# Kernel tuning notes

Measured on AMD Instinct MI355X. Metric: run time of the kernel, lower is better.

The kernel has to match this reference:

```python
import jax, jax.numpy as jnp
import numpy as np

B, T, HID = 2, 2048, 2048
NH, NKV, HD = 32, 8, 64
SCALE = HD ** -0.5
ROPE_THETA = 10000.0


def _rope_tables(key):
    # standard HF llama rope: cos/sin of shape [B, T, head_dim]
    inv_freq = 1.0 / (ROPE_THETA ** (jnp.arange(0, HD, 2, dtype=jnp.float32) / HD))
    pos = jnp.arange(T, dtype=jnp.float32)
    freqs = pos[:, None] * inv_freq[None, :]            # [T, HD/2]
    emb = jnp.concatenate([freqs, freqs], axis=-1)      # [T, HD]
    cos = jnp.broadcast_to(jnp.cos(emb)[None], (B, T, HD))
    sin = jnp.broadcast_to(jnp.sin(emb)[None], (B, T, HD))
    return cos, sin


def setup_inputs() -> dict:
    key = jax.random.key(0)
    ks = jax.random.split(key, 5)
    hidden_states = jax.random.normal(ks[0], (B, T, HID), dtype=jnp.float32)
    cos, sin = _rope_tables(key)
    s = 0.02
    wq = jax.random.normal(ks[1], (NH * HD, HID), dtype=jnp.float32) * s
    wk = jax.random.normal(ks[2], (NKV * HD, HID), dtype=jnp.float32) * s
    wv = jax.random.normal(ks[3], (NKV * HD, HID), dtype=jnp.float32) * s
    wo = jax.random.normal(ks[4], (HID, NH * HD), dtype=jnp.float32) * s
    return {"hidden_states": hidden_states, "cos": cos, "sin": sin,
            "wq": wq, "wk": wk, "wv": wv, "wo": wo}


def _rotate_half(x):
    x1, x2 = jnp.split(x, 2, axis=-1)
    return jnp.concatenate([-x2, x1], axis=-1)


def _apply_rope(q, k, cos, sin):
    # q: [B, NH, T, HD], k: [B, NKV, T, HD]; cos/sin: [B, T, HD] -> unsqueeze head dim
    c = cos[:, None, :, :]
    s = sin[:, None, :, :]
    q = q * c + _rotate_half(q) * s
    k = k * c + _rotate_half(k) * s
    return q, k


def reference(hidden_states, cos, sin, wq, wk, wv, wo):
    b, t, _ = hidden_states.shape
    # QKV projections (no bias, llama-style)
    q = (hidden_states @ wq.T).reshape(b, t, NH, HD).transpose(0, 2, 1, 3)    # [B,NH,T,HD]
    k = (hidden_states @ wk.T).reshape(b, t, NKV, HD).transpose(0, 2, 1, 3)   # [B,NKV,T,HD]
    v = (hidden_states @ wv.T).reshape(b, t, NKV, HD).transpose(0, 2, 1, 3)
    q, k = _apply_rope(q, k, cos, sin)
    # GQA: repeat kv heads
    rep = NH // NKV
    k = jnp.repeat(k, rep, axis=1)   # [B,NH,T,HD]
    v = jnp.repeat(v, rep, axis=1)
    # causal attention, scaling = head_dim**-0.5
    logits = jnp.einsum("bhqd,bhkd->bhqk", q, k) * SCALE
    causal = jnp.tril(jnp.ones((t, t), dtype=bool))
    logits = jnp.where(causal[None, None], logits, jnp.finfo(logits.dtype).min)
    probs = jax.nn.softmax(logits, axis=-1)
    attn = jnp.einsum("bhqk,bhkd->bhqd", probs, v)       # [B,NH,T,HD]
    attn = attn.transpose(0, 2, 1, 3).reshape(b, t, NH * HD)
    return attn @ wo.T
```

## Files before the change

### kernel.cpp

```cpp
#include <hip/hip_runtime.h>
#include <hip/hip_bf16.h>

#define T_SEQ 2048
#define HID_DIM 2048

typedef __attribute__((ext_vector_type(8))) short short8;
typedef __attribute__((ext_vector_type(4))) short short4v;
typedef __attribute__((ext_vector_type(4))) float f32x4;

#define MFMA16(a, b, c) __builtin_amdgcn_mfma_f32_16x16x32_bf16((a), (b), (c), 0, 0, 0)

static __device__ __forceinline__ ushort f2bf(float f) {
  union { __hip_bfloat16 h; ushort u; } un;
  un.h = __float2bfloat16(f);
  return un.u;
}
static __device__ __forceinline__ float bf2f(ushort u) {
  union { ushort u; __hip_bfloat16 h; } un;
  un.u = u;
  return __bfloat162float(un.h);
}

static __device__ __forceinline__ void gload_lds16(const void* g, void* l) {
  __builtin_amdgcn_global_load_lds(
      (const __attribute__((address_space(1))) void*)g,
      (__attribute__((address_space(3))) void*)l, 16, 0, 0);
}

__global__ __launch_bounds__(256) void cast_kernel(const float* __restrict__ in,
                                                   ushort* __restrict__ out, int n4) {
  int i = blockIdx.x * 256 + threadIdx.x;
  if (i >= n4) return;
  const float4 v = reinterpret_cast<const float4*>(in)[i];
  ushort4 o;
  o.x = f2bf(v.x); o.y = f2bf(v.y); o.z = f2bf(v.z); o.w = f2bf(v.w);
  reinterpret_cast<ushort4*>(out)[i] = o;
}

__device__ __forceinline__ void store_c(float* p, float v) { *p = v; }
__device__ __forceinline__ void store_c(ushort* p, float v) { *p = f2bf(v); }

template <int MODE, int BN, typename OutT>
__global__ __launch_bounds__(512) void gemm8p(const ushort* __restrict__ A,
                                              const ushort* __restrict__ W,
                                              OutT* __restrict__ C,
                                              ushort* __restrict__ vTout,
                                              int M, int N, int K) {
  constexpr int LA = 4;
  constexpr int LB = BN / 64;
  constexpr int NR = BN / 64;
  __shared__ __align__(16) ushort As[2][256 * 64];
  __shared__ __align__(16) ushort Bs[2][BN * 64];
  const int tid = threadIdx.x;
  const int lane = tid & 63, l15 = lane & 15, lhi = lane >> 4;
  const int wid = tid >> 6, wm = wid >> 2, wn = wid & 3;
  const int brow = blockIdx.y * 256, bcol = blockIdx.x * BN;
  const int nkt = K >> 6;

  const ushort* asrc[LA]; ushort* adst[LA];
#pragma unroll
  for (int j = 0; j < LA; ++j) {
    const int c = tid + 512 * j, row = c >> 3, k16 = c & 7;
    asrc[j] = A + (size_t)(brow + row) * K + ((k16 ^ (row & 7)) << 3);
    adst[j] = &As[0][0] + c * 8;
  }
  const ushort* bsrc[LB]; ushort* bdst[LB];
#pragma unroll
  for (int j = 0; j < LB; ++j) {
    const int c = tid + 512 * j, row = c >> 3, k16 = c & 7;
    bsrc[j] = W + (size_t)(bcol + row) * K + ((k16 ^ (row & 7)) << 3);
    bdst[j] = &Bs[0][0] + c * 8;
  }

#define STAGE8(kt_, bf_) do {                                              \
    _Pragma("unroll")                                                      \
    for (int j = 0; j < LA; ++j)                                           \
      gload_lds16(asrc[j] + (kt_) * 64, adst[j] + (bf_) * (256 * 64));     \
    _Pragma("unroll")                                                      \
    for (int j = 0; j < LB; ++j)                                           \
      gload_lds16(bsrc[j] + (kt_) * 64, bdst[j] + (bf_) * (BN * 64));      \
  } while (0)

  f32x4 acc[8][NR] = {};

  STAGE8(0, 0);
  for (int kt = 0; kt < nkt; ++kt) {
    const int bf = kt & 1;
    if (kt + 1 < nkt) {
      STAGE8(kt + 1, bf ^ 1);
      if constexpr (LA + LB == 8) asm volatile("s_waitcnt vmcnt(8)" ::: "memory");
      else                        asm volatile("s_waitcnt vmcnt(6)" ::: "memory");
    } else {
      asm volatile("s_waitcnt vmcnt(0)" ::: "memory");
    }
    __builtin_amdgcn_s_barrier();
    const char* abuf = (const char*)&As[bf][0];
    const char* bbuf = (const char*)&Bs[bf][0];
#pragma unroll
    for (int mh = 0; mh < 2; ++mh) {
      short8 af[4][2];
#pragma unroll
      for (int mi = 0; mi < 4; ++mi) {
        const int row = wm * 128 + (mh * 4 + mi) * 16 + l15;
        const int sw = (row & 7) << 4;
#pragma unroll
        for (int ks = 0; ks < 2; ++ks)
          af[mi][ks] = *(const short8*)(abuf + row * 128 + ((ks * 64 + lhi * 16) ^ sw));
      }
#pragma unroll
      for (int nh = 0; nh < NR / 2; ++nh) {
        short8 bfrag[2][2];
#pragma unroll
        for (int ni = 0; ni < 2; ++ni) {
          const int rowb = wn * (BN / 4) + (nh * 2 + ni) * 16 + l15;
          const int sw = (rowb & 7) << 4;
#pragma unroll
          for (int ks = 0; ks < 2; ++ks)
            bfrag[ni][ks] = *(const short8*)(bbuf + rowb * 128 + ((ks * 64 + lhi * 16) ^ sw));
        }
        __builtin_amdgcn_s_setprio(1);
#pragma unroll
        for (int ks = 0; ks < 2; ++ks)
#pragma unroll
          for (int mi = 0; mi < 4; ++mi)
#pragma unroll
            for (int ni = 0; ni < 2; ++ni)
              acc[mh * 4 + mi][nh * 2 + ni] =
                  MFMA16(af[mi][ks], bfrag[ni][ks], acc[mh * 4 + mi][nh * 2 + ni]);
        __builtin_amdgcn_s_setprio(0);
      }
    }
    __builtin_amdgcn_s_barrier();
  }
#undef STAGE8

  if (MODE == 2 && bcol >= 2560) {
#pragma unroll
    for (int mi8 = 0; mi8 < 8; ++mi8) {
      const int row = brow + wm * 128 + mi8 * 16 + lhi * 4;
      const int bb = row >> 11, t = row & 2047;
#pragma unroll
      for (int ni = 0; ni < NR; ++ni) {
        const int cv = bcol + wn * (BN / 4) + ni * 16 + l15 - 2560;
        const int hk = cv >> 6, dd = cv & 63;
        ushort4 o;
        o.x = f2bf(acc[mi8][ni][0]); o.y = f2bf(acc[mi8][ni][1]);
        o.z = f2bf(acc[mi8][ni][2]); o.w = f2bf(acc[mi8][ni][3]);
        *(ushort4*)&vTout[(size_t)((bb * 8 + hk) * 64 + dd) * 2048 + t] = o;
      }
    }
  } else {
    const int cstride = (MODE == 2) ? 2560 : N;
#pragma unroll
    for (int mi8 = 0; mi8 < 8; ++mi8) {
      const int row = brow + wm * 128 + mi8 * 16 + lhi * 4;
#pragma unroll
      for (int ni = 0; ni < NR; ++ni) {
        const int col = bcol + wn * (BN / 4) + ni * 16 + l15;
#pragma unroll
        for (int r = 0; r < 4; ++r)
          store_c(&C[(size_t)(row + r) * cstride + col], acc[mi8][ni][r]);
      }
    }
  }
}

__global__ __launch_bounds__(256) void rope_kernel(ushort* __restrict__ qkv,
                                                   const float* __restrict__ ct,
                                                   const float* __restrict__ st) {
  const int bt = blockIdx.x;
  ushort* row = qkv + (size_t)bt * 2560;
  const float* c = ct + (size_t)bt * 64;
  const float* s = st + (size_t)bt * 64;
  const int tid = threadIdx.x;
#pragma unroll
  for (int it = 0; it < 5; ++it) {
    const int idx = it * 256 + tid;
    const bool isQ = idx < 1024;
    const int sub = isQ ? idx : idx - 1024;
    const int hh = sub >> 5;
    const int p = sub & 31;
    const int col = (isQ ? 0 : 2048) + hh * 64 + p;
    const float x1 = bf2f(row[col]);
    const float x2 = bf2f(row[col + 32]);
    const float cc = c[p], ss = s[p];
    float y1 = x1 * cc - x2 * ss;
    float y2 = x2 * cc + x1 * ss;
    if (isQ) { y1 *= 0.125f; y2 *= 0.125f; }
    row[col] = f2bf(y1);
    row[col + 32] = f2bf(y2);
  }
}

#define PROCESS(SUF, diag_) do {                                              \
    f32x4 s_[4] = {};                                                         \
    __builtin_amdgcn_s_setprio(1);                                            \
    _Pragma("unroll")                                                         \
    for (int n = 0; n < 4; ++n) {                                             \
      const short8 k0_ = *(const short8*)(KtB + n * 2048 + base0);            \
      const short8 k1_ = *(const short8*)(KtB + n * 2048 + base1);            \
      s_[n] = MFMA16(k0_, q##SUF##0, s_[n]);                                  \
      s_[n] = MFMA16(k1_, q##SUF##1, s_[n]);                                  \
    }                                                                         \
    __builtin_amdgcn_s_setprio(0);                                            \
    if (diag_) {                                                              \
      _Pragma("unroll")                                                       \
      for (int n = 0; n < 4; ++n) {                                           \
        const int kb_ = 16 * n + 4 * lhi;                                     \
        _Pragma("unroll")                                                     \
        for (int r = 0; r < 4; ++r)                                           \
          if (kb_ + r > qloc) s_[n][r] = -1e30f;                              \
      }                                                                       \
    }                                                                         \
    float mx_;                                                                \
    {                                                                         \
      const float m0_ = fmaxf(fmaxf(s_[0][0], s_[0][1]), fmaxf(s_[0][2], s_[0][3])); \
      const float m1_ = fmaxf(fmaxf(s_[1][0], s_[1][1]), fmaxf(s_[1][2], s_[1][3])); \
      const float m2_ = fmaxf(fmaxf(s_[2][0], s_[2][1]), fmaxf(s_[2][2], s_[2][3])); \
      const float m3_ = fmaxf(fmaxf(s_[3][0], s_[3][1]), fmaxf(s_[3][2], s_[3][3])); \
      mx_ = fmaxf(fmaxf(m0_, m1_), fmaxf(m2_, m3_));                          \
    }                                                                         \
    mx_ = fmaxf(mx_, __shfl_xor(mx_, 16));                                    \
    mx_ = fmaxf(mx_, __shfl_xor(mx_, 32));                                    \
    const float mn_ = fmaxf(mS##SUF, mx_);                                    \
    const float al_ = __expf(mS##SUF - mn_);                                  \
    _Pragma("unroll")                                                         \
    for (int n = 0; n < 4; ++n) {                                             \
      s_[n][0] = __expf(s_[n][0] - mn_);                                      \
      s_[n][1] = __expf(s_[n][1] - mn_);                                      \
      s_[n][2] = __expf(s_[n][2] - mn_);                                      \
      s_[n][3] = __expf(s_[n][3] - mn_);                                      \
    }                                                                         \
    float rs_;                                                                \
    {                                                                         \
      const float t0_ = (s_[0][0] + s_[0][1]) + (s_[0][2] + s_[0][3]);        \
      const float t1_ = (s_[1][0] + s_[1][1]) + (s_[1][2] + s_[1][3]);        \
      const float t2_ = (s_[2][0] + s_[2][1]) + (s_[2][2] + s_[2][3]);        \
      const float t3_ = (s_[3][0] + s_[3][1]) + (s_[3][2] + s_[3][3]);        \
      rs_ = (t0_ + t1_) + (t2_ + t3_);                                        \
    }                                                                         \
    rs_ += __shfl_xor(rs_, 16);                                               \
    rs_ += __shfl_xor(rs_, 32);                                               \
    lS##SUF = lS##SUF * al_ + rs_;                                            \
    mS##SUF = mn_;                                                            \
    _Pragma("unroll")                                                         \
    for (int n = 0; n < 4; ++n) {                                             \
      short4v pk_;                                                            \
      pk_[0] = (short)f2bf(s_[n][0]);                                         \
      pk_[1] = (short)f2bf(s_[n][1]);                                         \
      pk_[2] = (short)f2bf(s_[n][2]);                                         \
      pk_[3] = (short)f2bf(s_[n][3]);                                         \
      *(short4v*)(PtB + prow + 32 * n + 8 * lhi) = pk_;                       \
    }                                                                         \
    const float al0_ = __shfl(al_, 4 * lhi + 0);                              \
    const float al1_ = __shfl(al_, 4 * lhi + 1);                              \
    const float al2_ = __shfl(al_, 4 * lhi + 2);                              \
    const float al3_ = __shfl(al_, 4 * lhi + 3);                              \
    _Pragma("unroll")                                                         \
    for (int n = 0; n < 4; ++n) {                                             \
      o##SUF[n][0] *= al0_;                                                   \
      o##SUF[n][1] *= al1_;                                                   \
      o##SUF[n][2] *= al2_;                                                   \
      o##SUF[n][3] *= al3_;                                                   \
    }                                                                         \
    {                                                                         \
      const short8 p0_ = *(const short8*)(PtB + prow + 16 * lhi);             \
      const short8 p1_ = *(const short8*)(PtB + prow + 64 + 16 * lhi);        \
      __builtin_amdgcn_s_setprio(1);                                          \
      _Pragma("unroll")                                                       \
      for (int n = 0; n < 4; ++n) {                                           \
        const short8 v0_ = *(const short8*)(VtB + n * 2048 + base0);          \
        const short8 v1_ = *(const short8*)(VtB + n * 2048 + base1);          \
        o##SUF[n] = MFMA16(p0_, v0_, o##SUF[n]);                              \
        o##SUF[n] = MFMA16(p1_, v1_, o##SUF[n]);                              \
      }                                                                       \
      __builtin_amdgcn_s_setprio(0);                                          \
    }                                                                         \
  } while (0)

__global__ __launch_bounds__(256) void attn_kernel(const ushort* __restrict__ qkv,
                                                   const ushort* __restrict__ vT,
                                                   ushort* __restrict__ out) {
  __shared__ __align__(16) ushort Kt[4096];
  __shared__ __align__(16) ushort Vt[4096];
  __shared__ __align__(16) ushort Pt[64 * 72];
  const int bid = blockIdx.x;
  const int j = bid >> 3;
  const int bh = (bid & 7) * 8 + (j & 7);
  const int bx = j >> 3;
  const int b = bh >> 5, h = bh & 31, hkv = h >> 2;
  const int tid = threadIdx.x;
  const int wid = tid >> 6, lane = tid & 63, l15 = lane & 15, lhi = lane >> 4;
  const int qA = bx, qB = 31 - bx;
  const int qloc = wid * 16 + l15;

  short8 qA0, qA1, qB0, qB1;
  {
    const size_t offA = (size_t)(b * T_SEQ + qA * 64 + qloc) * 2560 + h * 64;
    qA0 = *(const short8*)(qkv + offA + lhi * 8);
    qA1 = *(const short8*)(qkv + offA + 32 + lhi * 8);
    const size_t offB = (size_t)(b * T_SEQ + qB * 64 + qloc) * 2560 + h * 64;
    qB0 = *(const short8*)(qkv + offB + lhi * 8);
    qB1 = *(const short8*)(qkv + offB + 32 + lhi * 8);
  }

  f32x4 oA[4] = {}, oB[4] = {};
  float mSA = -1e30f, lSA = 0.f, mSB = -1e30f, lSB = 0.f;

  const int swb = (l15 & 7) << 4;
  const int base0 = l15 * 128 + ((lhi * 16) ^ swb);
  const int base1 = l15 * 128 + ((64 + lhi * 16) ^ swb);
  const char* KtB = (const char*)Kt;
  const char* VtB = (const char*)Vt;
  char* PtB = (char*)Pt;
  const int prow = qloc * 144;

  const int srow = tid >> 3, sgrp = tid & 7;
  const int d0s = ((sgrp ^ (srow & 7)) * 8);
  const ushort* kb_g = qkv + (size_t)b * T_SEQ * 2560 + 2048 + hkv * 64;
  const ushort* vb_g = vT + (size_t)(b * 8 + hkv) * 64 * 2048;
  ushort* ldsK = Kt + tid * 8;
  ushort* ldsV = Vt + tid * 8;

  for (int kt = 0; kt <= qB; ++kt) {
    const int ktb = kt * 64;
    gload_lds16(kb_g + (size_t)(ktb + srow) * 2560 + d0s, ldsK);
    gload_lds16(kb_g + (size_t)(ktb + 32 + srow) * 2560 + d0s, ldsK + 2048);
    gload_lds16(vb_g + (size_t)srow * 2048 + ktb + d0s, ldsV);
    gload_lds16(vb_g + (size_t)(32 + srow) * 2048 + ktb + d0s, ldsV + 2048);
    __syncthreads();
    PROCESS(B, kt == qB);
    if (kt <= qA) PROCESS(A, kt == qA);
    __syncthreads();
  }

  {
    const float invA = 1.f / lSA;
    const float i0 = __shfl(invA, 4 * lhi + 0), i1 = __shfl(invA, 4 * lhi + 1);
    const float i2 = __shfl(invA, 4 * lhi + 2), i3 = __shfl(invA, 4 * lhi + 3);
    const size_t orow = (size_t)(b * T_SEQ + qA * 64 + wid * 16 + lhi * 4);
#pragma unroll
    for (int n = 0; n < 4; ++n) {
      out[(orow + 0) * 2048 + h * 64 + n * 16 + l15] = f2bf(oA[n][0] * i0);
      out[(orow + 1) * 2048 + h * 64 + n * 16 + l15] = f2bf(oA[n][1] * i1);
      out[(orow + 2) * 2048 + h * 64 + n * 16 + l15] = f2bf(oA[n][2] * i2);
      out[(orow + 3) * 2048 + h * 64 + n * 16 + l15] = f2bf(oA[n][3] * i3);
    }
  }
  {
    const float invB = 1.f / lSB;
    const float i0 = __shfl(invB, 4 * lhi + 0), i1 = __shfl(invB, 4 * lhi + 1);
    const float i2 = __shfl(invB, 4 * lhi + 2), i3 = __shfl(invB, 4 * lhi + 3);
    const size_t orow = (size_t)(b * T_SEQ + qB * 64 + wid * 16 + lhi * 4);
#pragma unroll
    for (int n = 0; n < 4; ++n) {
      out[(orow + 0) * 2048 + h * 64 + n * 16 + l15] = f2bf(oB[n][0] * i0);
      out[(orow + 1) * 2048 + h * 64 + n * 16 + l15] = f2bf(oB[n][1] * i1);
      out[(orow + 2) * 2048 + h * 64 + n * 16 + l15] = f2bf(oB[n][2] * i2);
      out[(orow + 3) * 2048 + h * 64 + n * 16 + l15] = f2bf(oB[n][3] * i3);
    }
  }
}

extern "C" void kernel_launch(void* const* d_in, const int* in_sizes, int n_in,
                              void* d_out, int out_size, void* d_ws, size_t ws_size,
                              hipStream_t stream) {
  const float* hs   = (const float*)d_in[0];
  const float* cosb = (const float*)d_in[1];
  const float* sinb = (const float*)d_in[2];
  const float* wq   = (const float*)d_in[3];
  const float* wk   = (const float*)d_in[4];
  const float* wv   = (const float*)d_in[5];
  const float* wo   = (const float*)d_in[6];
  float* out = (float*)d_out;

  char* ws = (char*)d_ws;
  ushort* hsb   = (ushort*)(ws);
  ushort* wqkvb = (ushort*)(ws + 16777216);
  ushort* wob   = (ushort*)(ws + 29360128);
  ushort* qkvQK = (ushort*)(ws + 37748736);
  ushort* vTb   = (ushort*)(ws + 58720256);
  ushort* attno = hsb;

  cast_kernel<<<8192, 256, 0, stream>>>(hs, hsb, 2097152);
  cast_kernel<<<4096, 256, 0, stream>>>(wq, wqkvb, 1048576);
  cast_kernel<<<1024, 256, 0, stream>>>(wk, wqkvb + 4194304, 262144);
  cast_kernel<<<1024, 256, 0, stream>>>(wv, wqkvb + 5242880, 262144);
  cast_kernel<<<4096, 256, 0, stream>>>(wo, wob, 1048576);

  gemm8p<2, 256, ushort><<<dim3(12, 16), 512, 0, stream>>>(hsb, wqkvb, qkvQK,
                                                           vTb, 4096, 3072, 2048);

  rope_kernel<<<4096, 256, 0, stream>>>(qkvQK, cosb, sinb);

  attn_kernel<<<1024, 256, 0, stream>>>(qkvQK, vTb, attno);

  gemm8p<0, 128, float><<<dim3(16, 16), 512, 0, stream>>>(attno, wob, out,
                                                          nullptr, 4096, 2048, 2048);
}
```

Before: 341.3 us.

## Interleave GEMM prefetch across phases, double-buffer attention K/V, lazy softmax rescale

The GEMM now spreads next-tile global-to-LDS loads across the inner compute phases instead of issuing them all at once, and waits for all loads at the top of each iteration. The attention kernel double-buffers K/V tiles in LDS so the next tile's load overlaps the current tile's compute. It also skips the online-softmax rescale unless the running max grows by more than a threshold, and swizzles the P buffer to avoid LDS bank conflicts. The GEMM restructure drops the trailing barrier but adds a per-phase barrier and a vmcnt(0) wait. That may race, because buffer bufi^1 is overwritten while other waves may still be reading it. The lazy rescale relies on exp values staying bounded.

```diff
diff --git a/kernel.cpp b/kernel.cpp
--- a/kernel.cpp
+++ b/kernel.cpp
@@ -49,6 +49,8 @@
   constexpr int LA = 4;
   constexpr int LB = BN / 64;
   constexpr int NR = BN / 64;
+  constexpr int NPHT = 2 * (NR / 2);
+  constexpr int LPP = (LA + LB) / NPHT;
   __shared__ __align__(16) ushort As[2][256 * 64];
   __shared__ __align__(16) ushort Bs[2][BN * 64];
   const int tid = threadIdx.x;
@@ -72,67 +74,72 @@
     bdst[j] = &Bs[0][0] + c * 8;
   }
 
-#define STAGE8(kt_, bf_) do {                                              \
-    _Pragma("unroll")                                                      \
-    for (int j = 0; j < LA; ++j)                                           \
-      gload_lds16(asrc[j] + (kt_) * 64, adst[j] + (bf_) * (256 * 64));     \
-    _Pragma("unroll")                                                      \
-    for (int j = 0; j < LB; ++j)                                           \
-      gload_lds16(bsrc[j] + (kt_) * 64, bdst[j] + (bf_) * (BN * 64));      \
-  } while (0)
-
   f32x4 acc[8][NR] = {};
 
-  STAGE8(0, 0);
+#pragma unroll
+  for (int j = 0; j < LA; ++j) gload_lds16(asrc[j], adst[j]);
+#pragma unroll
+  for (int j = 0; j < LB; ++j) gload_lds16(bsrc[j], bdst[j]);
+
   for (int kt = 0; kt < nkt; ++kt) {
-    const int bf = kt & 1;
-    if (kt + 1 < nkt) {
-      STAGE8(kt + 1, bf ^ 1);
-      if constexpr (LA + LB == 8) asm volatile("s_waitcnt vmcnt(8)" ::: "memory");
-      else                        asm volatile("s_waitcnt vmcnt(6)" ::: "memory");
-    } else {
-      asm volatile("s_waitcnt vmcnt(0)" ::: "memory");
-    }
+    const int bufi = kt & 1;
+    asm volatile("s_waitcnt vmcnt(0)" ::: "memory");
     __builtin_amdgcn_s_barrier();
-    const char* abuf = (const char*)&As[bf][0];
-    const char* bbuf = (const char*)&Bs[bf][0];
+    const char* abuf = (const char*)&As[bufi][0];
+    const char* bbuf = (const char*)&Bs[bufi][0];
+    const bool pf = (kt + 1 < nkt);
 #pragma unroll
     for (int mh = 0; mh < 2; ++mh) {
-      short8 af[4][2];
-#pragma unroll
-      for (int mi = 0; mi < 4; ++mi) {
-        const int row = wm * 128 + (mh * 4 + mi) * 16 + l15;
-        const int sw = (row & 7) << 4;
+#pragma unroll
+      for (int nhh = 0; nhh < NR / 2; ++nhh) {
+        const int ph = mh * (NR / 2) + nhh;
+        if (pf) {
+#pragma unroll
+          for (int i = 0; i < LPP; ++i) {
+            const int f = ph * LPP + i;
+            if (f < LA)
+              gload_lds16(asrc[f] + (kt + 1) * 64,
+                          adst[f] + (bufi ^ 1) * (256 * 64));
+            else
+              gload_lds16(bsrc[f - LA] + (kt + 1) * 64,
+                          bdst[f - LA] + (bufi ^ 1) * (BN * 64));
+          }
+        }
+        short8 af_[4][2];
+#pragma unroll
+        for (int mi = 0; mi < 4; ++mi) {
+          const int row = wm * 128 + (mh * 4 + mi) * 16 + l15;
+          const int sw = (row & 7) << 4;
+#pragma unroll
+          for (int ks = 0; ks < 2; ++ks)
+            af_[mi][ks] = *(const short8*)(abuf + row * 128 +
+                                           ((ks * 64 + lhi * 16) ^ sw));
+        }
+        short8 bq_[2][2];
+#pragma unroll
+        for (int ni = 0; ni < 2; ++ni) {
+          const int rowb = wn * (BN / 4) + (nhh * 2 + ni) * 16 + l15;
+          const int sw = (rowb & 7) << 4;
+#pragma unroll
+          for (int ks = 0; ks < 2; ++ks)
+            bq_[ni][ks] = *(const short8*)(bbuf + rowb * 128 +
+                                           ((ks * 64 + lhi * 16) ^ sw));
+        }
+        __builtin_amdgcn_s_barrier();
+        __builtin_amdgcn_s_setprio(1);
 #pragma unroll
         for (int ks = 0; ks < 2; ++ks)
-          af[mi][ks] = *(const short8*)(abuf + row * 128 + ((ks * 64 + lhi * 16) ^ sw));
-      }
-#pragma unroll
-      for (int nh = 0; nh < NR / 2; ++nh) {
-        short8 bfrag[2][2];
-#pragma unroll
-        for (int ni = 0; ni < 2; ++ni) {
-          const int rowb = wn * (BN / 4) + (nh * 2 + ni) * 16 + l15;
-          const int sw = (rowb & 7) << 4;
-#pragma unroll
-          for (int ks = 0; ks < 2; ++ks)
-            bfrag[ni][ks] = *(const short8*)(bbuf + rowb * 128 + ((ks * 64 + lhi * 16) ^ sw));
-        }
-        __builtin_amdgcn_s_setprio(1);
-#pragma unroll
-        for (int ks = 0; ks < 2; ++ks)
 #pragma unroll
           for (int mi = 0; mi < 4; ++mi)
 #pragma unroll
             for (int ni = 0; ni < 2; ++ni)
-              acc[mh * 4 + mi][nh * 2 + ni] =
-                  MFMA16(af[mi][ks], bfrag[ni][ks], acc[mh * 4 + mi][nh * 2 + ni]);
+              acc[mh * 4 + mi][nhh * 2 + ni] =
+                  MFMA16(af_[mi][ks], bq_[ni][ks],
+                         acc[mh * 4 + mi][nhh * 2 + ni]);
         __builtin_amdgcn_s_setprio(0);
       }
     }
-    __builtin_amdgcn_s_barrier();
-  }
-#undef STAGE8
+  }
 
   if (MODE == 2 && bcol >= 2560) {
 #pragma unroll
@@ -197,8 +204,8 @@
     __builtin_amdgcn_s_setprio(1);                                            \
     _Pragma("unroll")                                                         \
     for (int n = 0; n < 4; ++n) {                                             \
-      const short8 k0_ = *(const short8*)(KtB + n * 2048 + base0);            \
-      const short8 k1_ = *(const short8*)(KtB + n * 2048 + base1);            \
+      const short8 k0_ = *(const short8*)(KtB + bfo_ + n * 2048 + base0);     \
+      const short8 k1_ = *(const short8*)(KtB + bfo_ + n * 2048 + base1);     \
       s_[n] = MFMA16(k0_, q##SUF##0, s_[n]);                                  \
       s_[n] = MFMA16(k1_, q##SUF##1, s_[n]);                                  \
     }                                                                         \
@@ -222,14 +229,29 @@
     }                                                                         \
     mx_ = fmaxf(mx_, __shfl_xor(mx_, 16));                                    \
     mx_ = fmaxf(mx_, __shfl_xor(mx_, 32));                                    \
-    const float mn_ = fmaxf(mS##SUF, mx_);                                    \
-    const float al_ = __expf(mS##SUF - mn_);                                  \
+    if (!__all(mx_ <= mS##SUF + 8.0f)) {      \
+      const float mn_ = fmaxf(mS##SUF, mx_);                                  \
+      const float al_ = __expf(mS##SUF - mn_);                                \
+      mS##SUF = mn_;                                                          \
+      lS##SUF *= al_;                                                         \
+      const float al0_ = __shfl(al_, 4 * lhi + 0);                            \
+      const float al1_ = __shfl(al_, 4 * lhi + 1);                            \
+      const float al2_ = __shfl(al_, 4 * lhi + 2);                            \
+      const float al3_ = __shfl(al_, 4 * lhi + 3);                            \
+      _Pragma("unroll")                                                       \
+      for (int n = 0; n < 4; ++n) {                                           \
+        o##SUF[n][0] *= al0_;                                                 \
+        o##SUF[n][1] *= al1_;                                                 \
+        o##SUF[n][2] *= al2_;                                                 \
+        o##SUF[n][3] *= al3_;                                                 \
+      }                                                                       \
+    }                                                                         \
     _Pragma("unroll")                                                         \
     for (int n = 0; n < 4; ++n) {                                             \
-      s_[n][0] = __expf(s_[n][0] - mn_);                                      \
-      s_[n][1] = __expf(s_[n][1] - mn_);                                      \
-      s_[n][2] = __expf(s_[n][2] - mn_);                                      \
-      s_[n][3] = __expf(s_[n][3] - mn_);                                      \
+      s_[n][0] = __expf(s_[n][0] - mS##SUF);                                  \
+      s_[n][1] = __expf(s_[n][1] - mS##SUF);                                  \
+      s_[n][2] = __expf(s_[n][2] - mS##SUF);                                  \
+      s_[n][3] = __expf(s_[n][3] - mS##SUF);                                  \
     }                                                                         \
     float rs_;                                                                \
     {                                                                         \
@@ -241,8 +263,7 @@
     }                                                                         \
     rs_ += __shfl_xor(rs_, 16);                                               \
     rs_ += __shfl_xor(rs_, 32);                                               \
-    lS##SUF = lS##SUF * al_ + rs_;                                            \
-    mS##SUF = mn_;                                                            \
+    lS##SUF += rs_;                                                           \
     _Pragma("unroll")                                                         \
     for (int n = 0; n < 4; ++n) {                                             \
       short4v pk_;                                                            \
@@ -250,27 +271,16 @@
       pk_[1] = (short)f2bf(s_[n][1]);                                         \
       pk_[2] = (short)f2bf(s_[n][2]);                                         \
       pk_[3] = (short)f2bf(s_[n][3]);                                         \
-      *(short4v*)(PtB + prow + 32 * n + 8 * lhi) = pk_;                       \
-    }                                                                         \
-    const float al0_ = __shfl(al_, 4 * lhi + 0);                              \
-    const float al1_ = __shfl(al_, 4 * lhi + 1);                              \
-    const float al2_ = __shfl(al_, 4 * lhi + 2);                              \
-    const float al3_ = __shfl(al_, 4 * lhi + 3);                              \
-    _Pragma("unroll")                                                         \
-    for (int n = 0; n < 4; ++n) {                                             \
-      o##SUF[n][0] *= al0_;                                                   \
-      o##SUF[n][1] *= al1_;                                                   \
-      o##SUF[n][2] *= al2_;                                                   \
-      o##SUF[n][3] *= al3_;                                                   \
+      *(short4v*)(PtB + prow + ((32 * n + 8 * lhi) ^ psw)) = pk_;             \
     }                                                                         \
     {                                                                         \
-      const short8 p0_ = *(const short8*)(PtB + prow + 16 * lhi);             \
-      const short8 p1_ = *(const short8*)(PtB + prow + 64 + 16 * lhi);        \
+      const short8 p0_ = *(const short8*)(PtB + prow + ((16 * lhi) ^ psw));   \
+      const short8 p1_ = *(const short8*)(PtB + prow + ((64 + 16 * lhi) ^ psw)); \
       __builtin_amdgcn_s_setprio(1);                                          \
       _Pragma("unroll")                                                       \
       for (int n = 0; n < 4; ++n) {                                           \
-        const short8 v0_ = *(const short8*)(VtB + n * 2048 + base0);          \
-        const short8 v1_ = *(const short8*)(VtB + n * 2048 + base1);          \
+        const short8 v0_ = *(const short8*)(VtB + bfo_ + n * 2048 + base0);   \
+        const short8 v1_ = *(const short8*)(VtB + bfo_ + n * 2048 + base1);   \
         o##SUF[n] = MFMA16(p0_, v0_, o##SUF[n]);                              \
         o##SUF[n] = MFMA16(p1_, v1_, o##SUF[n]);                              \
       }                                                                       \
@@ -281,9 +291,9 @@
 __global__ __launch_bounds__(256) void attn_kernel(const ushort* __restrict__ qkv,
                                                    const ushort* __restrict__ vT,
                                                    ushort* __restrict__ out) {
-  __shared__ __align__(16) ushort Kt[4096];
-  __shared__ __align__(16) ushort Vt[4096];
-  __shared__ __align__(16) ushort Pt[64 * 72];
+  __shared__ __align__(16) ushort Kt[2][4096];
+  __shared__ __align__(16) ushort Vt[2][4096];
+  __shared__ __align__(16) ushort Pt[4096];
   const int bid = blockIdx.x;
   const int j = bid >> 3;
   const int bh = (bid & 7) * 8 + (j & 7);
@@ -310,28 +320,43 @@
   const int swb = (l15 & 7) << 4;
   const int base0 = l15 * 128 + ((lhi * 16) ^ swb);
   const int base1 = l15 * 128 + ((64 + lhi * 16) ^ swb);
-  const char* KtB = (const char*)Kt;
-  const char* VtB = (const char*)Vt;
+  const char* KtB = (const char*)&Kt[0][0];
+  const char* VtB = (const char*)&Vt[0][0];
   char* PtB = (char*)Pt;
-  const int prow = qloc * 144;
+  const int prow = qloc * 128;
+  const int psw = (qloc & 7) << 4;
 
   const int srow = tid >> 3, sgrp = tid & 7;
   const int d0s = ((sgrp ^ (srow & 7)) * 8);
   const ushort* kb_g = qkv + (size_t)b * T_SEQ * 2560 + 2048 + hkv * 64;
   const ushort* vb_g = vT + (size_t)(b * 8 + hkv) * 64 * 2048;
-  ushort* ldsK = Kt + tid * 8;
-  ushort* ldsV = Vt + tid * 8;
+  ushort* ldsK = &Kt[0][0] + tid * 8;
+  ushort* ldsV = &Vt[0][0] + tid * 8;
+
+  gload_lds16(kb_g + (size_t)srow * 2560 + d0s, ldsK);
+  gload_lds16(kb_g + (size_t)(32 + srow) * 2560 + d0s, ldsK + 2048);
+  gload_lds16(vb_g + (size_t)srow * 2048 + d0s, ldsV);
+  gload_lds16(vb_g + (size_t)(32 + srow) * 2048 + d0s, ldsV + 2048);
 
   for (int kt = 0; kt <= qB; ++kt) {
-    const int ktb = kt * 64;
-    gload_lds16(kb_g + (size_t)(ktb + srow) * 2560 + d0s, ldsK);
-    gload_lds16(kb_g + (size_t)(ktb + 32 + srow) * 2560 + d0s, ldsK + 2048);
-    gload_lds16(vb_g + (size_t)srow * 2048 + ktb + d0s, ldsV);
-    gload_lds16(vb_g + (size_t)(32 + srow) * 2048 + ktb + d0s, ldsV + 2048);
-    __syncthreads();
+    const int bufi = kt & 1;
+    const int bfo_ = bufi << 13;
+    if (kt < qB) {
+      const int kt1 = (kt + 1) * 64;
+      ushort* dK = ldsK + (bufi ^ 1) * 4096;
+      ushort* dV = ldsV + (bufi ^ 1) * 4096;
+      gload_lds16(kb_g + (size_t)(kt1 + srow) * 2560 + d0s, dK);
+      gload_lds16(kb_g + (size_t)(kt1 + 32 + srow) * 2560 + d0s, dK + 2048);
+      gload_lds16(vb_g + (size_t)srow * 2048 + kt1 + d0s, dV);
+      gload_lds16(vb_g + (size_t)(32 + srow) * 2048 + kt1 + d0s, dV + 2048);
+      asm volatile("s_waitcnt vmcnt(4)" ::: "memory");
+    } else {
+      asm volatile("s_waitcnt vmcnt(0)" ::: "memory");
+    }
+    __builtin_amdgcn_s_barrier();
     PROCESS(B, kt == qB);
     if (kt <= qA) PROCESS(A, kt == qA);
-    __syncthreads();
+    __builtin_amdgcn_s_barrier();
   }
 
   {
```

Result: slower. 378.9 us (+11.0%).
